# Performance work log

Hardware: AMD Instinct MI355X
Metric: run time of the kernel (lower is better)

The kernel has to match this reference:

```python
import jax, jax.numpy as jnp
import numpy as np

N, E, DIN, H, C, OUT = 50000, 400000, 128, 4, 64, 40
HC = H * C
NEG_SLOPE = 0.2
EPS = 1e-5


def setup_inputs() -> dict:
    keys = iter(jax.random.split(jax.random.key(0), 64))
    def rn(shape, s=1.0):
        return jax.random.normal(next(keys), shape, jnp.float32) * s
    w = 0.05  # small init scale keeps activations stable through 3 layers
    inp = {}
    inp["x"] = rn((N, DIN))
    inp["src"] = jax.random.randint(next(keys), (E,), 0, N, jnp.int32)
    inp["dst"] = jax.random.randint(next(keys), (E,), 0, N, jnp.int32)
    # conv0: 128 -> (H=4, C=64), concat -> 256
    inp["Wl0"] = rn((DIN, HC), w); inp["bl0"] = jnp.zeros((HC,), jnp.float32)
    inp["Wr0"] = rn((DIN, HC), w); inp["br0"] = jnp.zeros((HC,), jnp.float32)
    inp["att0"] = rn((H, C), w);   inp["bc0"] = jnp.zeros((HC,), jnp.float32)
    inp["Ws0"] = rn((DIN, HC), w); inp["bs0"] = jnp.zeros((HC,), jnp.float32)
    inp["g0"] = jnp.ones((HC,), jnp.float32); inp["be0"] = jnp.zeros((HC,), jnp.float32)
    # conv1: 256 -> (4, 64), concat -> 256
    inp["Wl1"] = rn((HC, HC), w); inp["bl1"] = jnp.zeros((HC,), jnp.float32)
    inp["Wr1"] = rn((HC, HC), w); inp["br1"] = jnp.zeros((HC,), jnp.float32)
    inp["att1"] = rn((H, C), w);  inp["bc1"] = jnp.zeros((HC,), jnp.float32)
    inp["Ws1"] = rn((HC, HC), w); inp["bs1"] = jnp.zeros((HC,), jnp.float32)
    inp["g1"] = jnp.ones((HC,), jnp.float32); inp["be1"] = jnp.zeros((HC,), jnp.float32)
    # conv2: 256 -> (4, 40), mean over heads -> 40
    inp["Wl2"] = rn((HC, H * OUT), w); inp["bl2"] = jnp.zeros((H * OUT,), jnp.float32)
    inp["Wr2"] = rn((HC, H * OUT), w); inp["br2"] = jnp.zeros((H * OUT,), jnp.float32)
    inp["att2"] = rn((H, OUT), w);     inp["bc2"] = jnp.zeros((OUT,), jnp.float32)
    inp["Ws2"] = rn((HC, OUT), w);     inp["bs2"] = jnp.zeros((OUT,), jnp.float32)
    return inp


def _gatv2_conv(x, s, d, Wl, bl, Wr, br, att, bc, concat):
    # PyG GATv2Conv: lin_l on source, lin_r on target; e = LeakyReLU(xl_j + xr_i);
    # logit = <e, att>; softmax over edges sharing the same target; msg = xl_j.
    n = x.shape[0]
    h, c = att.shape
    xl = (x @ Wl + bl).reshape(n, h, c)
    xr = (x @ Wr + br).reshape(n, h, c)
    e = jax.nn.leaky_relu(xl[s] + xr[d], NEG_SLOPE)           # [E, H, C]
    logit = jnp.einsum("ehc,hc->eh", e, att)                  # [E, H]
    m = jax.ops.segment_max(logit, d, num_segments=n)          # per-target max
    a = jnp.exp(logit - m[d])
    z = jax.ops.segment_sum(a, d, num_segments=n)
    alpha = a / z[d]                                           # segment softmax
    out = jax.ops.segment_sum(alpha[:, :, None] * xl[s], d, num_segments=n)  # [N,H,C]
    out = out.reshape(n, h * c) if concat else out.mean(axis=1)
    return out + bc


def _bn(x, g, b):
    mu = x.mean(axis=0)
    var = x.var(axis=0)
    return g * (x - mu) / jnp.sqrt(var + EPS) + b


def reference(x, src, dst,
              Wl0, bl0, Wr0, br0, att0, bc0, Ws0, bs0, g0, be0,
              Wl1, bl1, Wr1, br1, att1, bc1, Ws1, bs1, g1, be1,
              Wl2, bl2, Wr2, br2, att2, bc2, Ws2, bs2):
    n = x.shape[0]
    loops = jnp.arange(n, dtype=src.dtype)  # add_self_loops=True (PyG default)
    s = jnp.concatenate([src, loops])
    d = jnp.concatenate([dst, loops])
    x1 = _gatv2_conv(x, s, d, Wl0, bl0, Wr0, br0, att0, bc0, True) + (x @ Ws0 + bs0)
    x1 = jax.nn.relu(_bn(x1, g0, be0))
    h = _gatv2_conv(x1, s, d, Wl1, bl1, Wr1, br1, att1, bc1, True) + (x1 @ Ws1 + bs1)
    x2 = jax.nn.relu(_bn(h, g1, be1))
    out = _gatv2_conv(x2, s, d, Wl2, bl2, Wr2, br2, att2, bc2, False) + (x2 @ Ws2 + bs2)
    return (h, out)
```

## Files before the change

### kernel.cpp

```cpp
#include <hip/hip_runtime.h>
#include <hip/hip_bf16.h>
#include <cstdint>
#include <cstddef>

#define DIN 128
#define HC 256
#define OUTC 40
#define HOUT 160
#define NEG 0.2f
#define BNEPS 1e-5f

typedef float f32x4 __attribute__((ext_vector_type(4)));
typedef __bf16 bf16x8 __attribute__((ext_vector_type(8)));

struct __align__(8) bh4 { __hip_bfloat16 x, y, z, w; };

__device__ __forceinline__ float4 ld4(const float* p) { return *(const float4*)p; }

__device__ __forceinline__ float4 ldb4(const __hip_bfloat16* p) {
    bh4 v = *(const bh4*)p;
    return make_float4(__bfloat162float(v.x), __bfloat162float(v.y),
                       __bfloat162float(v.z), __bfloat162float(v.w));
}

__device__ __forceinline__ void load_lds16(const void* g, void* l) {
    __builtin_amdgcn_global_load_lds((const __attribute__((address_space(1))) void*)g,
                                     (__attribute__((address_space(3))) void*)l, 16, 0, 0);
}

__global__ __launch_bounds__(256)
void gemm_mfma(const __hip_bfloat16* __restrict__ A, const __hip_bfloat16* __restrict__ Wt,
               const float* __restrict__ biasc, __hip_bfloat16* __restrict__ Y,
               int M, int K, int Npad, int gx, int q, int r) {
    __shared__ __hip_bfloat16 smem[128 * 136];
    __hip_bfloat16* As = smem;
    __hip_bfloat16* Bs = smem + 128 * 32;
    const int tid = threadIdx.x;
    const int lane = tid & 63, wid = tid >> 6;
    const int wm = wid >> 1, wn = wid & 1;

    const int orig = blockIdx.x;
    const int xcd = orig & 7, pos = orig >> 3;
    const int wgid = (xcd < r ? xcd * (q + 1) : r * (q + 1) + (xcd - r) * q) + pos;
    const int bn = (wgid % gx) * 128, bm = (wgid / gx) * 128;

    const int srow = lane >> 2;
    const int sseg = (lane & 3) * 8;
    f32x4 acc[4][4] = {};

    for (int k0 = 0; k0 < K; k0 += 32) {
#pragma unroll
        for (int i = 0; i < 2; ++i) {
            int c = 2 * wid + i;
            int ar = bm + 16 * c + srow; if (ar >= M) ar = M - 1;
            load_lds16(A + (size_t)ar * K + k0 + sseg, (char*)As + c * 1024);
            int br = bn + 16 * c + srow;
            load_lds16(Wt + (size_t)br * K + k0 + sseg, (char*)Bs + c * 1024);
        }
        __syncthreads();
        const int rkb = (lane >> 4) * 8;
        bf16x8 af[4], bfr[4];
#pragma unroll
        for (int i = 0; i < 4; ++i) {
            af[i]  = *(const bf16x8*)(As + (wm * 64 + i * 16 + (lane & 15)) * 32 + rkb);
            bfr[i] = *(const bf16x8*)(Bs + (wn * 64 + i * 16 + (lane & 15)) * 32 + rkb);
        }
#pragma unroll
        for (int mi = 0; mi < 4; ++mi)
#pragma unroll
            for (int ni = 0; ni < 4; ++ni)
                acc[mi][ni] = __builtin_amdgcn_mfma_f32_16x16x32_bf16(af[mi], bfr[ni], acc[mi][ni], 0, 0, 0);
        __syncthreads();
    }
    const int cl = lane & 15, rg4 = (lane >> 4) * 4;
#pragma unroll
    for (int ni = 0; ni < 4; ++ni) {
        float bv = biasc[bn + wn * 64 + ni * 16 + cl];
#pragma unroll
        for (int mi = 0; mi < 4; ++mi)
#pragma unroll
            for (int rr = 0; rr < 4; ++rr)
                smem[(wm * 64 + mi * 16 + rg4 + rr) * 136 + wn * 64 + ni * 16 + cl] =
                    __float2bfloat16(acc[mi][ni][rr] + bv);
    }
    __syncthreads();
#pragma unroll
    for (int it = 0; it < 8; ++it) {
        int row = it * 16 + (tid >> 4);
        int gm = bm + row;
        if (gm < M) {
            float4 v = *(const float4*)((const char*)(smem + row * 136) + (tid & 15) * 16);
            *(float4*)(Y + (size_t)gm * Npad + bn + (tid & 15) * 8) = v;
        }
    }
}

__global__ void prep_w_kernel(const float* __restrict__ W0, const float* __restrict__ b0, int n0,
                              const float* __restrict__ W1, const float* __restrict__ b1, int n1,
                              const float* __restrict__ W2, const float* __restrict__ b2, int n2,
                              int K, int Npad, __hip_bfloat16* __restrict__ Wt,
                              float* __restrict__ bc) {
    int idx = blockIdx.x * 256 + threadIdx.x;
    if (idx >= Npad * K) return;
    int n = idx / K, k = idx % K;
    float v = 0.f, bb = 0.f;
    if (n < n0)                { v = W0[(size_t)k * n0 + n];             bb = b0[n]; }
    else if (n < n0 + n1)      { v = W1[(size_t)k * n1 + (n - n0)];      bb = b1[n - n0]; }
    else if (n < n0 + n1 + n2) { v = W2[(size_t)k * n2 + (n - n0 - n1)]; bb = b2[n - n0 - n1]; }
    Wt[(size_t)n * K + k] = __float2bfloat16(v);
    if (k == 0) bc[n] = bb;
}

__global__ void f2b_kernel(const float* __restrict__ X, __hip_bfloat16* __restrict__ Y, int n4) {
    int i = blockIdx.x * 256 + threadIdx.x;
    if (i >= n4) return;
    float4 v = ((const float4*)X)[i];
    bh4 o;
    o.x = __float2bfloat16(v.x); o.y = __float2bfloat16(v.y);
    o.z = __float2bfloat16(v.z); o.w = __float2bfloat16(v.w);
    ((bh4*)Y)[i] = o;
}

__global__ void hist_kernel(const int* __restrict__ dst, int* __restrict__ deg, int E) {
    int e = blockIdx.x * 256 + threadIdx.x;
    if (e < E) atomicAdd(&deg[dst[e]], 1);
}

__global__ __launch_bounds__(256)
void scan1_kernel(int* __restrict__ a, int* __restrict__ bsum, int n) {
    const int tid = threadIdx.x;
    const int i = blockIdx.x * 256 + tid;
    const int lane = tid & 63, w = tid >> 6;
    int v = (i < n) ? (a[i] + 1) : 0;
    int x = v;
#pragma unroll
    for (int s = 1; s < 64; s <<= 1) { int t = __shfl_up(x, s); if (lane >= s) x += t; }
    __shared__ int ws[4];
    if (lane == 63) ws[w] = x;
    __syncthreads();
    int bo = 0;
    if (w > 0) bo = ws[0];
    if (w > 1) bo += ws[1];
    if (w > 2) bo += ws[2];
    if (i <= n) a[i] = bo + x - v;
    if (tid == 255) bsum[blockIdx.x] = bo + x;
}

__global__ __launch_bounds__(256)
void scan2_kernel(int* __restrict__ bsum, int nb) {
    const int tid = threadIdx.x;
    const int lane = tid & 63, w = tid >> 6;
    int v = (tid < nb) ? bsum[tid] : 0;
    int x = v;
#pragma unroll
    for (int s = 1; s < 64; s <<= 1) { int t = __shfl_up(x, s); if (lane >= s) x += t; }
    __shared__ int ws[4];
    if (lane == 63) ws[w] = x;
    __syncthreads();
    int bo = 0;
    if (w > 0) bo = ws[0];
    if (w > 1) bo += ws[1];
    if (w > 2) bo += ws[2];
    if (tid < nb) bsum[tid] = bo + x - v;
}

__global__ void scan3_kernel(int* __restrict__ a, const int* __restrict__ bsum, int n) {
    int i = blockIdx.x * 256 + threadIdx.x;
    if (i <= n) a[i] += bsum[blockIdx.x];
}

__global__ void scatter_kernel(const int* __restrict__ src, const int* __restrict__ dst,
                               const int* __restrict__ off, int* __restrict__ cursor,
                               int* __restrict__ srcs, int E, int N) {
    int e = blockIdx.x * 256 + threadIdx.x;
    if (e >= E + N) return;
    int s, d;
    if (e < E) { s = src[e]; d = dst[e]; }
    else       { s = e - E;  d = e - E; }
    int p = atomicAdd(&cursor[d], 1);
    srcs[off[d] + p] = s;
}

__device__ __forceinline__ float edge_logit(const float4& xl, const float4& xr, const float4& av) {
    float ex = xl.x + xr.x; ex = ex > 0.f ? ex : NEG * ex;
    float ey = xl.y + xr.y; ey = ey > 0.f ? ey : NEG * ey;
    float ez = xl.z + xr.z; ez = ez > 0.f ? ez : NEG * ez;
    float ew = xl.w + xr.w; ew = ew > 0.f ? ew : NEG * ew;
    float p = ex * av.x + ey * av.y + ez * av.z + ew * av.w;
    p += __shfl_xor(p, 1);
    p += __shfl_xor(p, 2);
    p += __shfl_xor(p, 4);
    p += __shfl_xor(p, 8);
    return fminf(p, 50.f);
}

__global__ __launch_bounds__(256)
void gat_conv_cat(const __hip_bfloat16* __restrict__ XL, const __hip_bfloat16* __restrict__ XR,
                  const __hip_bfloat16* __restrict__ SK, const float* __restrict__ att,
                  const float* __restrict__ bc,
                  const int* __restrict__ off, const int* __restrict__ srcs,
                  float* __restrict__ OUT, int N, int RS) {
    int n = blockIdx.x * 4 + (threadIdx.x >> 6);
    if (n >= N) return;
    int lane = threadIdx.x & 63;
    int c4 = lane << 2;
    const float4 xr = ldb4(XR + (size_t)n * RS + c4);
    const float4 av = ld4(att + c4);
    float z = 0.f;
    float ax = 0.f, ay = 0.f, az = 0.f, aw = 0.f;
    int j = off[n];
    const int e1 = off[n + 1];
    for (; j + 3 < e1; j += 4) {
        int s0 = srcs[j], s1 = srcs[j + 1], s2 = srcs[j + 2], s3 = srcs[j + 3];
        float4 xl0 = ldb4(XL + (size_t)s0 * RS + c4);
        float4 xl1 = ldb4(XL + (size_t)s1 * RS + c4);
        float4 xl2 = ldb4(XL + (size_t)s2 * RS + c4);
        float4 xl3 = ldb4(XL + (size_t)s3 * RS + c4);
        float a0 = __expf(edge_logit(xl0, xr, av));
        float a1 = __expf(edge_logit(xl1, xr, av));
        float a2 = __expf(edge_logit(xl2, xr, av));
        float a3 = __expf(edge_logit(xl3, xr, av));
        z += a0; ax += a0 * xl0.x; ay += a0 * xl0.y; az += a0 * xl0.z; aw += a0 * xl0.w;
        z += a1; ax += a1 * xl1.x; ay += a1 * xl1.y; az += a1 * xl1.z; aw += a1 * xl1.w;
        z += a2; ax += a2 * xl2.x; ay += a2 * xl2.y; az += a2 * xl2.z; aw += a2 * xl2.w;
        z += a3; ax += a3 * xl3.x; ay += a3 * xl3.y; az += a3 * xl3.z; aw += a3 * xl3.w;
    }
    for (; j < e1; ++j) {
        int s0 = srcs[j];
        float4 xl0 = ldb4(XL + (size_t)s0 * RS + c4);
        float a0 = __expf(edge_logit(xl0, xr, av));
        z += a0; ax += a0 * xl0.x; ay += a0 * xl0.y; az += a0 * xl0.z; aw += a0 * xl0.w;
    }
    float inv = 1.f / z;
    float4 sk = ldb4(SK + (size_t)n * RS + c4);
    float4 bb = ld4(bc + c4);
    float4 r;
    r.x = ax * inv + bb.x + sk.x;
    r.y = ay * inv + bb.y + sk.y;
    r.z = az * inv + bb.z + sk.z;
    r.w = aw * inv + bb.w + sk.w;
    *(float4*)(OUT + (size_t)n * HC + c4) = r;
}

__device__ __forceinline__ void mean_edge(const __hip_bfloat16* __restrict__ XL, size_t srow,
                                          int bm_ch, int bt_ch,
                                          const float4& xr4, float xrt,
                                          const float4& av4, float avt,
                                          float& z, float& c0, float& c1, float& c2,
                                          float& c3, float& c4) {
    float4 x4 = ldb4(XL + srow + bm_ch);
    float xt = __bfloat162float(XL[srow + bt_ch]);
    float e0 = x4.x + xr4.x; e0 = e0 > 0.f ? e0 : NEG * e0;
    float e1 = x4.y + xr4.y; e1 = e1 > 0.f ? e1 : NEG * e1;
    float e2 = x4.z + xr4.z; e2 = e2 > 0.f ? e2 : NEG * e2;
    float e3 = x4.w + xr4.w; e3 = e3 > 0.f ? e3 : NEG * e3;
    float et = xt + xrt;     et = et > 0.f ? et : NEG * et;
    float p = e0 * av4.x + e1 * av4.y + e2 * av4.z + e3 * av4.w + et * avt;
    p += __shfl_xor(p, 1);
    p += __shfl_xor(p, 2);
    p += __shfl_xor(p, 4);
    p = fminf(p, 50.f);
    float a = __expf(p);
    z += a;
    c0 += a * x4.x; c1 += a * x4.y; c2 += a * x4.z; c3 += a * x4.w; c4 += a * xt;
}

__global__ __launch_bounds__(256)
void gat_conv_mean(const __hip_bfloat16* __restrict__ XL, const __hip_bfloat16* __restrict__ XR,
                   const __hip_bfloat16* __restrict__ SK, const float* __restrict__ att,
                   const float* __restrict__ bc,
                   const int* __restrict__ off, const int* __restrict__ srcs,
                   float* __restrict__ OUT, int N, int RS) {
    const int lane = threadIdx.x & 63;
    const int half = lane >> 5, sub = lane & 31;
    const int n = blockIdx.x * 8 + (threadIdx.x >> 6) * 2 + half;
    if (n >= N) return;
    const int hd = sub >> 3, q = sub & 7;
    const int bm_ch = hd * OUTC + q * 4;
    const int bt_ch = hd * OUTC + 32 + q;
    const size_t nrow = (size_t)n * RS;
    const float4 xr4 = ldb4(XR + nrow + bm_ch);
    const float xrt = __bfloat162float(XR[nrow + bt_ch]);
    const float4 av4 = ld4(att + bm_ch);
    const float avt = att[bt_ch];
    float z = 0.f, c0 = 0.f, c1 = 0.f, c2 = 0.f, c3 = 0.f, c4 = 0.f;
    int j = off[n];
    const int e1 = off[n + 1];
    for (; j + 3 < e1; j += 4) {
        size_t r0 = (size_t)srcs[j] * RS,     r1 = (size_t)srcs[j + 1] * RS;
        size_t r2 = (size_t)srcs[j + 2] * RS, r3 = (size_t)srcs[j + 3] * RS;
        mean_edge(XL, r0, bm_ch, bt_ch, xr4, xrt, av4, avt, z, c0, c1, c2, c3, c4);
        mean_edge(XL, r1, bm_ch, bt_ch, xr4, xrt, av4, avt, z, c0, c1, c2, c3, c4);
        mean_edge(XL, r2, bm_ch, bt_ch, xr4, xrt, av4, avt, z, c0, c1, c2, c3, c4);
        mean_edge(XL, r3, bm_ch, bt_ch, xr4, xrt, av4, avt, z, c0, c1, c2, c3, c4);
    }
    for (; j < e1; ++j)
        mean_edge(XL, (size_t)srcs[j] * RS, bm_ch, bt_ch, xr4, xrt, av4, avt, z, c0, c1, c2, c3, c4);

    float inv = 1.f / z;
    float r0 = c0 * inv, r1 = c1 * inv, r2 = c2 * inv, r3 = c3 * inv, r4 = c4 * inv;
    r0 += __shfl_xor(r0, 8); r0 += __shfl_xor(r0, 16);
    r1 += __shfl_xor(r1, 8); r1 += __shfl_xor(r1, 16);
    r2 += __shfl_xor(r2, 8); r2 += __shfl_xor(r2, 16);
    r3 += __shfl_xor(r3, 8); r3 += __shfl_xor(r3, 16);
    r4 += __shfl_xor(r4, 8); r4 += __shfl_xor(r4, 16);
    if (hd == 0) {
        int o = q << 2;
        float4 sk4 = ldb4(SK + nrow + o);
        float skt = __bfloat162float(SK[nrow + 32 + q]);
        float4 rv;
        rv.x = r0 * 0.25f + bc[o + 0] + sk4.x;
        rv.y = r1 * 0.25f + bc[o + 1] + sk4.y;
        rv.z = r2 * 0.25f + bc[o + 2] + sk4.z;
        rv.w = r3 * 0.25f + bc[o + 3] + sk4.w;
        *(float4*)(OUT + (size_t)n * OUTC + o) = rv;
        OUT[(size_t)n * OUTC + 32 + q] = r4 * 0.25f + bc[32 + q] + skt;
    }
}

__global__ __launch_bounds__(256)
void bn_stats_kernel(const float* __restrict__ X, float* __restrict__ sums,
                     float* __restrict__ sqs, int N) {
    int c = threadIdx.x;
    float s = 0.f, qq = 0.f;
    for (int n = blockIdx.x; n < N; n += gridDim.x) {
        float v = X[(size_t)n * HC + c];
        s += v; qq += v * v;
    }
    atomicAdd(&sums[c], s);
    atomicAdd(&sqs[c], qq);
}

__global__ __launch_bounds__(256)
void bn_finalize_kernel(const float* __restrict__ sums, const float* __restrict__ sqs,
                        const float* __restrict__ g, const float* __restrict__ be,
                        float* __restrict__ scale, float* __restrict__ shift, int N) {
    int c = threadIdx.x;
    float mean = sums[c] / (float)N;
    float var = sqs[c] / (float)N - mean * mean;
    float inv = rsqrtf(var + BNEPS);
    float sc = g[c] * inv;
    scale[c] = sc;
    shift[c] = be[c] - mean * sc;
}

__global__ __launch_bounds__(256)
void bn_apply_relu_kernel(const float* __restrict__ X, const float* __restrict__ sc,
                          const float* __restrict__ sh, __hip_bfloat16* __restrict__ Y, int n4) {
    for (int i = blockIdx.x * blockDim.x + threadIdx.x; i < n4; i += gridDim.x * blockDim.x) {
        int c4 = (i & 63) << 2;
        float4 v = ((const float4*)X)[i];
        float4 s = ld4(sc + c4);
        float4 h = ld4(sh + c4);
        bh4 r;
        r.x = __float2bfloat16(fmaxf(v.x * s.x + h.x, 0.f));
        r.y = __float2bfloat16(fmaxf(v.y * s.y + h.y, 0.f));
        r.z = __float2bfloat16(fmaxf(v.z * s.z + h.z, 0.f));
        r.w = __float2bfloat16(fmaxf(v.w * s.w + h.w, 0.f));
        ((bh4*)Y)[i] = r;
    }
}

extern "C" void kernel_launch(void* const* d_in, const int* in_sizes, int n_in,
                              void* d_out, int out_size, void* d_ws, size_t ws_size,
                              hipStream_t stream) {
    const int N = in_sizes[0] / DIN;
    const int E = in_sizes[1];
    const int Et = E + N;

    const float* x   = (const float*)d_in[0];
    const int* src   = (const int*)d_in[1];
    const int* dst   = (const int*)d_in[2];
    const float* Wl0 = (const float*)d_in[3];  const float* bl0 = (const float*)d_in[4];
    const float* Wr0 = (const float*)d_in[5];  const float* br0 = (const float*)d_in[6];
    const float* att0= (const float*)d_in[7];  const float* bc0 = (const float*)d_in[8];
    const float* Ws0 = (const float*)d_in[9];  const float* bs0 = (const float*)d_in[10];
    const float* g0  = (const float*)d_in[11]; const float* be0 = (const float*)d_in[12];
    const float* Wl1 = (const float*)d_in[13]; const float* bl1 = (const float*)d_in[14];
    const float* Wr1 = (const float*)d_in[15]; const float* br1 = (const float*)d_in[16];
    const float* att1= (const float*)d_in[17]; const float* bc1 = (const float*)d_in[18];
    const float* Ws1 = (const float*)d_in[19]; const float* bs1 = (const float*)d_in[20];
    const float* g1  = (const float*)d_in[21]; const float* be1 = (const float*)d_in[22];
    const float* Wl2 = (const float*)d_in[23]; const float* bl2 = (const float*)d_in[24];
    const float* Wr2 = (const float*)d_in[25]; const float* br2 = (const float*)d_in[26];
    const float* att2= (const float*)d_in[27]; const float* bc2 = (const float*)d_in[28];
    const float* Ws2 = (const float*)d_in[29]; const float* bs2 = (const float*)d_in[30];

    float* outh = (float*)d_out;
    float* outy = outh + (size_t)N * HC;

    __hip_bfloat16* Y  = (__hip_bfloat16*)d_ws;
    __hip_bfloat16* xb = Y + (size_t)N * 768;
    __hip_bfloat16* Wt = xb + (size_t)N * HC;
    float* bcc  = (float*)(Wt + 768 * 256);
    int* off    = (int*)(bcc + 768);
    int* cursor = off + (N + 1);
    int* srcs   = cursor + N;
    int* bsum   = srcs + Et;
    float* bn   = (float*)((((uintptr_t)(bsum + 256)) + 15) & ~(uintptr_t)15);

    const int nb_scan = (N + 1 + 255) / 256;
    hipMemsetAsync(off, 0, (size_t)(N + 1) * sizeof(int), stream);
    hipMemsetAsync(cursor, 0, (size_t)N * sizeof(int), stream);
    hist_kernel<<<(E + 255) / 256, 256, 0, stream>>>(dst, off, E);
    scan1_kernel<<<nb_scan, 256, 0, stream>>>(off, bsum, N);
    scan2_kernel<<<1, 256, 0, stream>>>(bsum, nb_scan);
    scan3_kernel<<<nb_scan, 256, 0, stream>>>(off, bsum, N);
    scatter_kernel<<<(Et + 255) / 256, 256, 0, stream>>>(src, dst, off, cursor, srcs, E, N);

    const int gmy = (N + 127) / 128;
    const int convGrid = (N + 3) / 4;
    const int meanGrid = (N + 7) / 8;
    const int nwgA = 6 * gmy, qA = nwgA / 8, rA = nwgA % 8;
    const int nwgC = 3 * gmy, qC = nwgC / 8, rC = nwgC % 8;

    f2b_kernel<<<(N * DIN / 4 + 255) / 256, 256, 0, stream>>>(x, xb, N * DIN / 4);
    prep_w_kernel<<<(768 * DIN + 255) / 256, 256, 0, stream>>>(
        Wl0, bl0, HC, Wr0, br0, HC, Ws0, bs0, HC, DIN, 768, Wt, bcc);
    gemm_mfma<<<nwgA, 256, 0, stream>>>(xb, Wt, bcc, Y, N, DIN, 768, 6, qA, rA);
    gat_conv_cat<<<convGrid, 256, 0, stream>>>(Y, Y + 256, Y + 512, att0, bc0, off, srcs,
                                               outh, N, 768);
    hipMemsetAsync(bn, 0, 512 * sizeof(float), stream);
    bn_stats_kernel<<<1024, 256, 0, stream>>>(outh, bn, bn + 256, N);
    bn_finalize_kernel<<<1, 256, 0, stream>>>(bn, bn + 256, g0, be0, bn + 512, bn + 768, N);
    bn_apply_relu_kernel<<<2048, 256, 0, stream>>>(outh, bn + 512, bn + 768, xb, N * (HC / 4));

    prep_w_kernel<<<(768 * HC + 255) / 256, 256, 0, stream>>>(
        Wl1, bl1, HC, Wr1, br1, HC, Ws1, bs1, HC, HC, 768, Wt, bcc);
    gemm_mfma<<<nwgA, 256, 0, stream>>>(xb, Wt, bcc, Y, N, HC, 768, 6, qA, rA);
    gat_conv_cat<<<convGrid, 256, 0, stream>>>(Y, Y + 256, Y + 512, att1, bc1, off, srcs,
                                               outh, N, 768);
    hipMemsetAsync(bn, 0, 512 * sizeof(float), stream);
    bn_stats_kernel<<<1024, 256, 0, stream>>>(outh, bn, bn + 256, N);
    bn_finalize_kernel<<<1, 256, 0, stream>>>(bn, bn + 256, g1, be1, bn + 512, bn + 768, N);
    bn_apply_relu_kernel<<<2048, 256, 0, stream>>>(outh, bn + 512, bn + 768, xb, N * (HC / 4));

    prep_w_kernel<<<(384 * HC + 255) / 256, 256, 0, stream>>>(
        Wl2, bl2, HOUT, Wr2, br2, HOUT, Ws2, bs2, OUTC, HC, 384, Wt, bcc);
    gemm_mfma<<<nwgC, 256, 0, stream>>>(xb, Wt, bcc, Y, N, HC, 384, 3, qC, rC);
    gat_conv_mean<<<meanGrid, 256, 0, stream>>>(Y, Y + 160, Y + 320, att2, bc2, off, srcs,
                                                outy, N, 384);
}
```

Measured before the change: 427.7 us.

## Fuse BatchNorm statistics into GAT conv epilogue and shrink GEMM LDS

Measured after the change: 1.102 ms. +157.7%, slower.

```diff
diff --git a/kernel.cpp b/kernel.cpp
--- a/kernel.cpp
+++ b/kernel.cpp
@@ -32,9 +32,9 @@
 void gemm_mfma(const __hip_bfloat16* __restrict__ A, const __hip_bfloat16* __restrict__ Wt,
                const float* __restrict__ biasc, __hip_bfloat16* __restrict__ Y,
                int M, int K, int Npad, int gx, int q, int r) {
-    __shared__ __hip_bfloat16 smem[128 * 136];
+    __shared__ __hip_bfloat16 smem[64 * 136];
     __hip_bfloat16* As = smem;
-    __hip_bfloat16* Bs = smem + 128 * 32;
+    __hip_bfloat16* Bs = smem + 4096;
     const int tid = threadIdx.x;
     const int lane = tid & 63, wid = tid >> 6;
     const int wm = wid >> 1, wn = wid & 1;
@@ -74,24 +74,30 @@
     }
     const int cl = lane & 15, rg4 = (lane >> 4) * 4;
 #pragma unroll
-    for (int ni = 0; ni < 4; ++ni) {
-        float bv = biasc[bn + wn * 64 + ni * 16 + cl];
-#pragma unroll
-        for (int mi = 0; mi < 4; ++mi)
-#pragma unroll
-            for (int rr = 0; rr < 4; ++rr)
-                smem[(wm * 64 + mi * 16 + rg4 + rr) * 136 + wn * 64 + ni * 16 + cl] =
-                    __float2bfloat16(acc[mi][ni][rr] + bv);
-    }
-    __syncthreads();
-#pragma unroll
-    for (int it = 0; it < 8; ++it) {
-        int row = it * 16 + (tid >> 4);
-        int gm = bm + row;
-        if (gm < M) {
-            float4 v = *(const float4*)((const char*)(smem + row * 136) + (tid & 15) * 16);
-            *(float4*)(Y + (size_t)gm * Npad + bn + (tid & 15) * 8) = v;
-        }
+    for (int h = 0; h < 2; ++h) {
+        if (wm == h) {
+#pragma unroll
+            for (int ni = 0; ni < 4; ++ni) {
+                float bv = biasc[bn + wn * 64 + ni * 16 + cl];
+#pragma unroll
+                for (int mi = 0; mi < 4; ++mi)
+#pragma unroll
+                    for (int rr = 0; rr < 4; ++rr)
+                        smem[(mi * 16 + rg4 + rr) * 136 + wn * 64 + ni * 16 + cl] =
+                            __float2bfloat16(acc[mi][ni][rr] + bv);
+            }
+        }
+        __syncthreads();
+#pragma unroll
+        for (int it = 0; it < 4; ++it) {
+            int row = it * 16 + (tid >> 4);
+            int gm = bm + h * 64 + row;
+            if (gm < M) {
+                float4 v = *(const float4*)((const char*)(smem + row * 136) + (tid & 15) * 16);
+                *(float4*)(Y + (size_t)gm * Npad + bn + (tid & 15) * 8) = v;
+            }
+        }
+        __syncthreads();
     }
 }
 
@@ -194,52 +200,81 @@
     return fminf(p, 50.f);
 }
 
-__global__ __launch_bounds__(256)
-void gat_conv_cat(const __hip_bfloat16* __restrict__ XL, const __hip_bfloat16* __restrict__ XR,
-                  const __hip_bfloat16* __restrict__ SK, const float* __restrict__ att,
-                  const float* __restrict__ bc,
-                  const int* __restrict__ off, const int* __restrict__ srcs,
-                  float* __restrict__ OUT, int N, int RS) {
-    int n = blockIdx.x * 4 + (threadIdx.x >> 6);
-    if (n >= N) return;
-    int lane = threadIdx.x & 63;
-    int c4 = lane << 2;
-    const float4 xr = ldb4(XR + (size_t)n * RS + c4);
+template<bool BF16OUT>
+__global__ __launch_bounds__(256)
+void gat_conv_cat_f(const __hip_bfloat16* __restrict__ XL, const __hip_bfloat16* __restrict__ XR,
+                    const __hip_bfloat16* __restrict__ SK, const float* __restrict__ att,
+                    const float* __restrict__ bc,
+                    const int* __restrict__ off, const int* __restrict__ srcs,
+                    void* __restrict__ OUTv, float* __restrict__ sums, float* __restrict__ sqs,
+                    int N, int RS) {
+    const int lane = threadIdx.x & 63, wid = threadIdx.x >> 6;
+    const int c4 = lane << 2;
     const float4 av = ld4(att + c4);
-    float z = 0.f;
-    float ax = 0.f, ay = 0.f, az = 0.f, aw = 0.f;
-    int j = off[n];
-    const int e1 = off[n + 1];
-    for (; j + 3 < e1; j += 4) {
-        int s0 = srcs[j], s1 = srcs[j + 1], s2 = srcs[j + 2], s3 = srcs[j + 3];
-        float4 xl0 = ldb4(XL + (size_t)s0 * RS + c4);
-        float4 xl1 = ldb4(XL + (size_t)s1 * RS + c4);
-        float4 xl2 = ldb4(XL + (size_t)s2 * RS + c4);
-        float4 xl3 = ldb4(XL + (size_t)s3 * RS + c4);
-        float a0 = __expf(edge_logit(xl0, xr, av));
-        float a1 = __expf(edge_logit(xl1, xr, av));
-        float a2 = __expf(edge_logit(xl2, xr, av));
-        float a3 = __expf(edge_logit(xl3, xr, av));
-        z += a0; ax += a0 * xl0.x; ay += a0 * xl0.y; az += a0 * xl0.z; aw += a0 * xl0.w;
-        z += a1; ax += a1 * xl1.x; ay += a1 * xl1.y; az += a1 * xl1.z; aw += a1 * xl1.w;
-        z += a2; ax += a2 * xl2.x; ay += a2 * xl2.y; az += a2 * xl2.z; aw += a2 * xl2.w;
-        z += a3; ax += a3 * xl3.x; ay += a3 * xl3.y; az += a3 * xl3.z; aw += a3 * xl3.w;
-    }
-    for (; j < e1; ++j) {
-        int s0 = srcs[j];
-        float4 xl0 = ldb4(XL + (size_t)s0 * RS + c4);
-        float a0 = __expf(edge_logit(xl0, xr, av));
-        z += a0; ax += a0 * xl0.x; ay += a0 * xl0.y; az += a0 * xl0.z; aw += a0 * xl0.w;
-    }
-    float inv = 1.f / z;
-    float4 sk = ldb4(SK + (size_t)n * RS + c4);
-    float4 bb = ld4(bc + c4);
-    float4 r;
-    r.x = ax * inv + bb.x + sk.x;
-    r.y = ay * inv + bb.y + sk.y;
-    r.z = az * inv + bb.z + sk.z;
-    r.w = aw * inv + bb.w + sk.w;
-    *(float4*)(OUT + (size_t)n * HC + c4) = r;
+    const float4 bb = ld4(bc + c4);
+    f32x4 msum = {0.f, 0.f, 0.f, 0.f}, msq = {0.f, 0.f, 0.f, 0.f};
+
+#pragma unroll
+    for (int it = 0; it < 4; ++it) {
+        int n = blockIdx.x * 16 + wid * 4 + it;
+        if (n < N) {
+            const float4 xr = ldb4(XR + (size_t)n * RS + c4);
+            float z = 0.f, ax = 0.f, ay = 0.f, az = 0.f, aw = 0.f;
+            int j = off[n];
+            const int e1 = off[n + 1];
+            for (; j + 3 < e1; j += 4) {
+                int s0 = srcs[j], s1 = srcs[j + 1], s2 = srcs[j + 2], s3 = srcs[j + 3];
+                float4 xl0 = ldb4(XL + (size_t)s0 * RS + c4);
+                float4 xl1 = ldb4(XL + (size_t)s1 * RS + c4);
+                float4 xl2 = ldb4(XL + (size_t)s2 * RS + c4);
+                float4 xl3 = ldb4(XL + (size_t)s3 * RS + c4);
+                float a0 = __expf(edge_logit(xl0, xr, av));
+                float a1 = __expf(edge_logit(xl1, xr, av));
+                float a2 = __expf(edge_logit(xl2, xr, av));
+                float a3 = __expf(edge_logit(xl3, xr, av));
+                z += a0; ax += a0 * xl0.x; ay += a0 * xl0.y; az += a0 * xl0.z; aw += a0 * xl0.w;
+                z += a1; ax += a1 * xl1.x; ay += a1 * xl1.y; az += a1 * xl1.z; aw += a1 * xl1.w;
+                z += a2; ax += a2 * xl2.x; ay += a2 * xl2.y; az += a2 * xl2.z; aw += a2 * xl2.w;
+                z += a3; ax += a3 * xl3.x; ay += a3 * xl3.y; az += a3 * xl3.z; aw += a3 * xl3.w;
+            }
+            for (; j < e1; ++j) {
+                int s0 = srcs[j];
+                float4 xl0 = ldb4(XL + (size_t)s0 * RS + c4);
+                float a0 = __expf(edge_logit(xl0, xr, av));
+                z += a0; ax += a0 * xl0.x; ay += a0 * xl0.y; az += a0 * xl0.z; aw += a0 * xl0.w;
+            }
+            float inv = 1.f / z;
+            float4 sk = ldb4(SK + (size_t)n * RS + c4);
+            float rx = ax * inv + bb.x + sk.x;
+            float ry = ay * inv + bb.y + sk.y;
+            float rz = az * inv + bb.z + sk.z;
+            float rw = aw * inv + bb.w + sk.w;
+            msum[0] += rx; msum[1] += ry; msum[2] += rz; msum[3] += rw;
+            msq[0] += rx * rx; msq[1] += ry * ry; msq[2] += rz * rz; msq[3] += rw * rw;
+            if (BF16OUT) {
+                bh4 o;
+                o.x = __float2bfloat16(rx); o.y = __float2bfloat16(ry);
+                o.z = __float2bfloat16(rz); o.w = __float2bfloat16(rw);
+                *((bh4*)OUTv + (size_t)n * (HC / 4) + lane) = o;
+            } else {
+                float4 o = make_float4(rx, ry, rz, rw);
+                *((float4*)OUTv + (size_t)n * (HC / 4) + lane) = o;
+            }
+        }
+    }
+    __shared__ f32x4 ssum[4][64], ssq[4][64];
+    ssum[wid][lane] = msum;
+    ssq[wid][lane] = msq;
+    __syncthreads();
+    if (wid == 0) {
+        f32x4 s = ssum[0][lane] + ssum[1][lane] + ssum[2][lane] + ssum[3][lane];
+        f32x4 qq = ssq[0][lane] + ssq[1][lane] + ssq[2][lane] + ssq[3][lane];
+#pragma unroll
+        for (int i = 0; i < 4; ++i) {
+            atomicAdd(&sums[c4 + i], s[i]);
+            atomicAdd(&sqs[c4 + i], qq[i]);
+        }
+    }
 }
 
 __device__ __forceinline__ void mean_edge(const __hip_bfloat16* __restrict__ XL, size_t srow,
@@ -319,19 +354,6 @@
 }
 
 __global__ __launch_bounds__(256)
-void bn_stats_kernel(const float* __restrict__ X, float* __restrict__ sums,
-                     float* __restrict__ sqs, int N) {
-    int c = threadIdx.x;
-    float s = 0.f, qq = 0.f;
-    for (int n = blockIdx.x; n < N; n += gridDim.x) {
-        float v = X[(size_t)n * HC + c];
-        s += v; qq += v * v;
-    }
-    atomicAdd(&sums[c], s);
-    atomicAdd(&sqs[c], qq);
-}
-
-__global__ __launch_bounds__(256)
 void bn_finalize_kernel(const float* __restrict__ sums, const float* __restrict__ sqs,
                         const float* __restrict__ g, const float* __restrict__ be,
                         float* __restrict__ scale, float* __restrict__ shift, int N) {
@@ -345,11 +367,28 @@
 }
 
 __global__ __launch_bounds__(256)
-void bn_apply_relu_kernel(const float* __restrict__ X, const float* __restrict__ sc,
-                          const float* __restrict__ sh, __hip_bfloat16* __restrict__ Y, int n4) {
+void bn_apply_relu_f(const float* __restrict__ X, const float* __restrict__ sc,
+                     const float* __restrict__ sh, __hip_bfloat16* __restrict__ Y, int n4) {
     for (int i = blockIdx.x * blockDim.x + threadIdx.x; i < n4; i += gridDim.x * blockDim.x) {
         int c4 = (i & 63) << 2;
         float4 v = ((const float4*)X)[i];
+        float4 s = ld4(sc + c4);
+        float4 h = ld4(sh + c4);
+        bh4 r;
+        r.x = __float2bfloat16(fmaxf(v.x * s.x + h.x, 0.f));
+        r.y = __float2bfloat16(fmaxf(v.y * s.y + h.y, 0.f));
+        r.z = __float2bfloat16(fmaxf(v.z * s.z + h.z, 0.f));
+        r.w = __float2bfloat16(fmaxf(v.w * s.w + h.w, 0.f));
+        ((bh4*)Y)[i] = r;
+    }
+}
+
+__global__ __launch_bounds__(256)
+void bn_apply_relu_b(const __hip_bfloat16* __restrict__ X, const float* __restrict__ sc,
+                     const float* __restrict__ sh, __hip_bfloat16* __restrict__ Y, int n4) {
+    for (int i = blockIdx.x * blockDim.x + threadIdx.x; i < n4; i += gridDim.x * blockDim.x) {
+        int c4 = (i & 63) << 2;
+        float4 v = ldb4(X + (size_t)i * 4);
         float4 s = ld4(sc + c4);
         float4 h = ld4(sh + c4);
         bh4 r;
@@ -398,10 +437,10 @@
     int* srcs   = cursor + N;
     int* bsum   = srcs + Et;
     float* bn   = (float*)((((uintptr_t)(bsum + 256)) + 15) & ~(uintptr_t)15);
+    __hip_bfloat16* P = (__hip_bfloat16*)(bn + 1024);
 
     const int nb_scan = (N + 1 + 255) / 256;
-    hipMemsetAsync(off, 0, (size_t)(N + 1) * sizeof(int), stream);
-    hipMemsetAsync(cursor, 0, (size_t)N * sizeof(int), stream);
+    hipMemsetAsync(off, 0, (size_t)(2 * N + 1) * sizeof(int), stream);
     hist_kernel<<<(E + 255) / 256, 256, 0, stream>>>(dst, off, E);
     scan1_kernel<<<nb_scan, 256, 0, stream>>>(off, bsum, N);
     scan2_kernel<<<1, 256, 0, stream>>>(bsum, nb_scan);
@@ -409,7 +448,7 @@
     scatter_kernel<<<(Et + 255) / 256, 256, 0, stream>>>(src, dst, off, cursor, srcs, E, N);
 
     const int gmy = (N + 127) / 128;
-    const int convGrid = (N + 3) / 4;
+    const int catGrid = (N + 15) / 16;
     const int meanGrid = (N + 7) / 8;
     const int nwgA = 6 * gmy, qA = nwgA / 8, rA = nwgA % 8;
     const int nwgC = 3 * gmy, qC = nwgC / 8, rC = nwgC % 8;
@@ -418,22 +457,20 @@
     prep_w_kernel<<<(768 * DIN + 255) / 256, 256, 0, stream>>>(
         Wl0, bl0, HC, Wr0, br0, HC, Ws0, bs0, HC, DIN, 768, Wt, bcc);
     gemm_mfma<<<nwgA, 256, 0, stream>>>(xb, Wt, bcc, Y, N, DIN, 768, 6, qA, rA);
-    gat_conv_cat<<<convGrid, 256, 0, stream>>>(Y, Y + 256, Y + 512, att0, bc0, off, srcs,
-                                               outh, N, 768);
     hipMemsetAsync(bn, 0, 512 * sizeof(float), stream);
-    bn_stats_kernel<<<1024, 256, 0, stream>>>(outh, bn, bn + 256, N);
+    gat_conv_cat_f<true><<<catGrid, 256, 0, stream>>>(Y, Y + 256, Y + 512, att0, bc0,
+                                                      off, srcs, P, bn, bn + 256, N, 768);
     bn_finalize_kernel<<<1, 256, 0, stream>>>(bn, bn + 256, g0, be0, bn + 512, bn + 768, N);
-    bn_apply_relu_kernel<<<2048, 256, 0, stream>>>(outh, bn + 512, bn + 768, xb, N * (HC / 4));
+    bn_apply_relu_b<<<2048, 256, 0, stream>>>(P, bn + 512, bn + 768, xb, N * (HC / 4));
 
     prep_w_kernel<<<(768 * HC + 255) / 256, 256, 0, stream>>>(
         Wl1, bl1, HC, Wr1, br1, HC, Ws1, bs1, HC, HC, 768, Wt, bcc);
     gemm_mfma<<<nwgA, 256, 0, stream>>>(xb, Wt, bcc, Y, N, HC, 768, 6, qA, rA);
-    gat_conv_cat<<<convGrid, 256, 0, stream>>>(Y, Y + 256, Y + 512, att1, bc1, off, srcs,
-                                               outh, N, 768);
     hipMemsetAsync(bn, 0, 512 * sizeof(float), stream);
-    bn_stats_kernel<<<1024, 256, 0, stream>>>(outh, bn, bn + 256, N);
+    gat_conv_cat_f<false><<<catGrid, 256, 0, stream>>>(Y, Y + 256, Y + 512, att1, bc1,
+                                                       off, srcs, outh, bn, bn + 256, N, 768);
     bn_finalize_kernel<<<1, 256, 0, stream>>>(bn, bn + 256, g1, be1, bn + 512, bn + 768, N);
-    bn_apply_relu_kernel<<<2048, 256, 0, stream>>>(outh, bn + 512, bn + 768, xb, N * (HC / 4));
+    bn_apply_relu_f<<<2048, 256, 0, stream>>>(outh, bn + 512, bn + 768, xb, N * (HC / 4));
 
     prep_w_kernel<<<(384 * HC + 255) / 256, 256, 0, stream>>>(
         Wl2, bl2, HOUT, Wr2, br2, HOUT, Ws2, bs2, OUTC, HC, 384, Wt, bcc);
```
